# Performance work log

Measured on AMD Instinct MI355X. Metric: run time of the kernel, lower is better.

Reference implementation:

```python
import jax, jax.numpy as jnp
import numpy as np

N_FREQ = 7  # freqs = 2**linspace(0, 6, 7) == 2**arange(7)
SKIP = (4,)


def nerf_encode(p):
    # nerfstudio NeRFEncoding with include_input=True, windows_param=None
    freqs = 2.0 ** jnp.arange(N_FREQ, dtype=p.dtype)          # [7]
    scaled = (2.0 * jnp.pi) * p                               # [N,3]
    s = (scaled[..., None] * freqs).reshape(p.shape[0], -1)   # [N,21]
    enc = jnp.sin(jnp.concatenate([s, s + 0.5 * jnp.pi], axis=-1))  # [N,42] = sin | cos
    return jnp.concatenate([enc, p], axis=-1)                 # [N,45]


def _hat_pt3d(w):
    # pytorch3d hat convention (transpose of the standard skew matrix)
    x, y, z = w[:, 0], w[:, 1], w[:, 2]
    o = jnp.zeros_like(x)
    return jnp.stack([
        jnp.stack([o, z, -y], -1),
        jnp.stack([-z, o, x], -1),
        jnp.stack([y, -x, o], -1)], -2)                       # [N,3,3]


def se3_exp_map_T(screw, eps=1e-4):
    # pytorch3d.transforms.se3_exp_map(screw).permute(0, 2, 1)
    v, w = screw[:, :3], screw[:, 3:]
    ang2 = jnp.clip(jnp.sum(w * w, axis=-1), eps, None)
    ang = jnp.sqrt(ang2)
    K = _hat_pt3d(w)
    KK = jnp.matmul(K, K)
    f1 = (jnp.sin(ang) / ang)[:, None, None]
    f2 = ((1.0 - jnp.cos(ang)) / ang2)[:, None, None]
    f3 = ((ang - jnp.sin(ang)) / (ang * ang2))[:, None, None]
    I = jnp.eye(3, dtype=screw.dtype)
    R = I + f1 * K + f2 * KK       # pytorch3d (row-vector) rotation
    V = I + f2 * K + f3 * KK
    T = jnp.einsum('nij,nj->ni', V, v)
    M = jnp.zeros((screw.shape[0], 4, 4), screw.dtype)
    M = M.at[:, :3, :3].set(jnp.swapaxes(R, -1, -2))  # transpose of [[R,0],[T,1]]
    M = M.at[:, :3, 3].set(T)
    M = M.at[:, 3, 3].set(1.0)
    return M


def mlp_stem(x, Ws, bs):
    inp = x
    n = len(Ws)
    for i in range(n):
        if i in SKIP:
            x = jnp.concatenate([inp, x], axis=-1)
        x = x @ Ws[i].T + bs[i]
        x = jax.nn.relu(x)  # hidden activation; i==n-1 is out_activation (also ReLU)
    return x


def setup_inputs() -> dict:
    key = jax.random.key(0)
    ks = jax.random.split(key, 16)
    N = 524288
    d = {
        'positions': jax.random.uniform(ks[0], (N, 3), jnp.float32),
        'directions': jax.random.normal(ks[1], (N, 3), jnp.float32),
        'warp_code': jax.random.normal(ks[2], (N, 8), jnp.float32),
    }
    fan_ins = [53, 128, 128, 128, 181, 128]
    for i, fi in enumerate(fan_ins):
        d[f'W{i}'] = jax.random.normal(ks[3 + i], (128, fi), jnp.float32) / np.sqrt(fi)
        d[f'b{i}'] = jnp.zeros((128,), jnp.float32)
    d['Wr'] = jax.random.normal(ks[10], (3, 128), jnp.float32) * 1e-5
    d['br'] = jnp.zeros((3,), jnp.float32)
    d['Wv'] = jax.random.normal(ks[11], (3, 128), jnp.float32) * 1e-5
    d['bv'] = jnp.zeros((3,), jnp.float32)
    return d


def reference(positions, directions, warp_code,
              W0, b0, W1, b1, W2, b2, W3, b3, W4, b4, W5, b5,
              Wr, br, Wv, bv):
    enc = nerf_encode(positions)                                  # [N,45]
    feat = mlp_stem(jnp.concatenate([enc, warp_code], axis=-1),
                    [W0, W1, W2, W3, W4, W5], [b0, b1, b2, b3, b4, b5])  # [N,128]
    r = feat @ Wr.T + br                                          # [N,3]
    v = feat @ Wv.T + bv                                          # [N,3]
    screw = jnp.concatenate([v, r], axis=-1)                      # [N,6]
    M = se3_exp_map_T(screw)                                      # [N,4,4]
    ph = jnp.concatenate([positions, jnp.ones_like(positions[:, :1])], axis=-1)
    wp_h = jnp.einsum('nij,nj->ni', M, ph)                        # [N,4]
    wp = wp_h[:, :3] / wp_h[:, 3:]
    wp = jnp.where(jnp.isnan(wp), positions, wp)
    rots = M[:, :3, :3]
    wd = jnp.einsum('nij,nj->ni', rots, directions)
    wd = jnp.where(jnp.isnan(wd), directions, wd)
    return wp, wd
```

## Files before the change

kernel.cpp:

```cpp
#include <hip/hip_runtime.h>
#include <hip/hip_bf16.h>
#include <math.h>


typedef __bf16 bf16x8 __attribute__((ext_vector_type(8)));
typedef float  f32x4  __attribute__((ext_vector_type(4)));

#define NROWS 524288
#define BROWS 128

#define P0 0
#define P1 8192
#define P2 24576
#define P3 40960
#define P4 57344
#define P5 81920
#define PH 98304
#define PTOT 100352

#define X0_OFF   0
#define XA_OFF   16384
#define BIAS_OFF 49152
#define SC_OFF   0
#define LDS_SZ   52352

template<int KS, int FAN>
__device__ __forceinline__ float pack_val(const float* __restrict__ W, int idx)
{
    int f  = idx / (KS * 512);
    int r2 = idx % (KS * 512);
    int s  = r2 >> 9, r3 = r2 & 511, ln = r3 >> 3, j = r3 & 7;
    int col = f * 16 + (ln & 15);
    int k   = s * 32 + (ln >> 4) * 8 + j;
    if (FAN == 128) return W[col * 128 + k];
    if (FAN == 53)  return (k < 53) ? W[col * 53 + k] : 0.f;
    if (k < 53)  return W[col * 181 + k];
    if (k < 64)  return 0.f;
    return W[col * 181 + (k - 11)];
}

__global__ void pack_w(const float* __restrict__ W0, const float* __restrict__ W1,
                       const float* __restrict__ W2, const float* __restrict__ W3,
                       const float* __restrict__ W4, const float* __restrict__ W5,
                       const float* __restrict__ Wr, const float* __restrict__ Wv,
                       __bf16* __restrict__ pk)
{
    int e = blockIdx.x * 256 + threadIdx.x;
    if (e >= PTOT) return;
    float val;
    if (e >= PH) {
        int rem = e - PH;
        int s = rem >> 9, r3 = rem & 511, ln = r3 >> 3, j = r3 & 7;
        int col = ln & 15;
        int k = s * 32 + (ln >> 4) * 8 + j;
        if (col < 3)      val = Wv[col * 128 + k];
        else if (col < 6) val = Wr[(col - 3) * 128 + k];
        else              val = 0.f;
    }
    else if (e < P1) val = pack_val<2, 53 >(W0, e - P0);
    else if (e < P2) val = pack_val<4, 128>(W1, e - P1);
    else if (e < P3) val = pack_val<4, 128>(W2, e - P2);
    else if (e < P4) val = pack_val<4, 128>(W3, e - P3);
    else if (e < P5) val = pack_val<6, 181>(W4, e - P4);
    else             val = pack_val<4, 128>(W5, e - P5);
    pk[e] = (__bf16)val;
}

__device__ __forceinline__ unsigned pack_bf16_2(float a, float b) {
    union { __bf16 h; unsigned short u; } x, y;
    x.h = (__bf16)a; y.h = (__bf16)b;
    return ((unsigned)y.u << 16) | (unsigned)x.u;
}

template<int KS, int SPLIT, bool BAR1>
__device__ __forceinline__ void mlp_layer(unsigned char* smem,
    const __bf16* __restrict__ pkL, int lyr,
    int lane, int c, int g, int mfG, int nfG)
{
    f32x4 acc[2][4];
    #pragma unroll
    for (int mf = 0; mf < 2; mf++) {
        f32x4 bb = *(const f32x4*)(smem + BIAS_OFF
                                   + (lyr * 128 + mfG * 32 + mf * 16 + g * 4) * 4);
        #pragma unroll
        for (int nf = 0; nf < 4; nf++) acc[mf][nf] = bb;
    }

    const bf16x8* pW = (const bf16x8*)pkL;
    bf16x8 Wf[2][2];
    #pragma unroll
    for (int mf = 0; mf < 2; mf++)
        Wf[0][mf] = pW[((mfG * 2 + mf) * KS + 0) * 64 + lane];

    #pragma unroll
    for (int s = 0; s < KS; s++) {
        if (s + 1 < KS) {
            #pragma unroll
            for (int mf = 0; mf < 2; mf++)
                Wf[(s + 1) & 1][mf] = pW[((mfG * 2 + mf) * KS + (s + 1)) * 64 + lane];
        }
        bf16x8 Bf[4];
        {
            int base, stride, k0;
            if (s < SPLIT) { base = X0_OFF; stride = 128; k0 = s * 32; }
            else           { base = XA_OFF; stride = 256; k0 = (s - SPLIT) * 32; }
            int bc = 2 * k0 + 16 * g;
            #pragma unroll
            for (int nf = 0; nf < 4; nf++) {
                int row = nfG * 64 + nf * 16 + c;
                Bf[nf] = *(const bf16x8*)(smem + base + row * stride
                                          + (bc ^ ((row & 7) << 4)));
            }
        }
        #pragma unroll
        for (int mf = 0; mf < 2; mf++)
            #pragma unroll
            for (int nf = 0; nf < 4; nf++)
                acc[mf][nf] = __builtin_amdgcn_mfma_f32_16x16x32_bf16(
                    Wf[s & 1][mf], Bf[nf], acc[mf][nf], 0, 0, 0);
    }

    if (BAR1) __syncthreads();

    #pragma unroll
    for (int mf = 0; mf < 2; mf++)
        #pragma unroll
        for (int nf = 0; nf < 4; nf++) {
            int row = nfG * 64 + nf * 16 + c;
            int bc  = 64 * mfG + 32 * mf + 8 * g;
            f32x4 a = acc[mf][nf];
            uint2 wv;
            wv.x = pack_bf16_2(fmaxf(a[0], 0.f), fmaxf(a[1], 0.f));
            wv.y = pack_bf16_2(fmaxf(a[2], 0.f), fmaxf(a[3], 0.f));
            *(uint2*)(smem + XA_OFF + row * 256 + (bc ^ ((row & 7) << 4))) = wv;
        }
    __syncthreads();
}

__global__ __launch_bounds__(512, 6)
void se3_fused(const float* __restrict__ pos, const float* __restrict__ dir,
               const float* __restrict__ wcode,
               const float* __restrict__ b0, const float* __restrict__ b1,
               const float* __restrict__ b2, const float* __restrict__ b3,
               const float* __restrict__ b4, const float* __restrict__ b5,
               const float* __restrict__ br, const float* __restrict__ bv,
               const __bf16* __restrict__ pk,
               float* __restrict__ out)
{
    __shared__ unsigned char smem[LDS_SZ];
    const int tid  = threadIdx.x;
    const int lane = tid & 63;
    const int w    = tid >> 6;
    const int c    = lane & 15;
    const int g    = lane >> 4;
    const int mfG  = w & 3;
    const int nfG  = w >> 2;
    const int r0   = blockIdx.x * BROWS;

    if (tid < 256) {
        int row = tid >> 1, h = tid & 1;
        int gg = r0 + row;
        float p0 = pos[gg*3+0], p1 = pos[gg*3+1], p2 = pos[gg*3+2];
        float vals[32];
        if (h == 0) {
            #pragma unroll
            for (int j = 0; j < 21; j++) {
                float p = (j < 7) ? p0 : (j < 14 ? p1 : p2);
                float t = p * (float)(1 << (j % 7));
                t -= floorf(t);
                vals[j] = __sinf(6.283185307179586f * t);
            }
            #pragma unroll
            for (int j = 21; j < 32; j++) {
                int idx = j - 21;
                float p = (idx < 7) ? p0 : (idx < 14 ? p1 : p2);
                float t = p * (float)(1 << (idx % 7));
                t -= floorf(t);
                vals[j] = __cosf(6.283185307179586f * t);
            }
        } else {
            #pragma unroll
            for (int j = 0; j < 10; j++) {
                int idx = 11 + j;
                float p = (idx < 14) ? p1 : p2;
                float t = p * (float)(1 << (idx % 7));
                t -= floorf(t);
                vals[j] = __cosf(6.283185307179586f * t);
            }
            vals[10] = p0; vals[11] = p1; vals[12] = p2;
            const float4* wc4 = (const float4*)(wcode + (size_t)gg * 8);
            float4 wa = wc4[0], wb = wc4[1];
            vals[13] = wa.x; vals[14] = wa.y; vals[15] = wa.z; vals[16] = wa.w;
            vals[17] = wb.x; vals[18] = wb.y; vals[19] = wb.z; vals[20] = wb.w;
            #pragma unroll
            for (int j = 21; j < 32; j++) vals[j] = 0.f;
        }
        unsigned pkd[16];
        #pragma unroll
        for (int i = 0; i < 16; i++) pkd[i] = pack_bf16_2(vals[2*i], vals[2*i+1]);
        unsigned char* base = smem + X0_OFF + row * 128;
        int sw = (row & 7) << 4;
        #pragma unroll
        for (int cc = 0; cc < 4; cc++) {
            uint4 wv; wv.x = pkd[4*cc]; wv.y = pkd[4*cc+1];
            wv.z = pkd[4*cc+2]; wv.w = pkd[4*cc+3];
            *(uint4*)(base + ((64 * h + 16 * cc) ^ sw)) = wv;
        }
    } else {
        for (int i = tid - 256; i < 800; i += 256) {
            float v;
            if (i < 768) {
                int l = i >> 7, m = i & 127;
                const float* bp = (l == 0) ? b0 : (l == 1) ? b1 : (l == 2) ? b2
                               : (l == 3) ? b3 : (l == 4) ? b4 : b5;
                v = bp[m];
            } else {
                int m = i - 768;
                v = (m < 3) ? bv[m] : ((m < 6) ? br[m - 3] : 0.f);
            }
            *(float*)(smem + BIAS_OFF + i * 4) = v;
        }
    }
    __syncthreads();

    mlp_layer<2,2,false>(smem, pk + P0, 0, lane, c, g, mfG, nfG);
    mlp_layer<4,0,true >(smem, pk + P1, 1, lane, c, g, mfG, nfG);
    mlp_layer<4,0,true >(smem, pk + P2, 2, lane, c, g, mfG, nfG);
    mlp_layer<4,0,true >(smem, pk + P3, 3, lane, c, g, mfG, nfG);
    mlp_layer<6,2,true >(smem, pk + P4, 4, lane, c, g, mfG, nfG);
    mlp_layer<4,0,true >(smem, pk + P5, 5, lane, c, g, mfG, nfG);

    if (mfG == 0) {
        const bf16x8* pW = (const bf16x8*)(pk + PH);
        f32x4 hb = *(const f32x4*)(smem + BIAS_OFF + (768 + g * 4) * 4);
        f32x4 hacc[4];
        #pragma unroll
        for (int nf = 0; nf < 4; nf++) hacc[nf] = hb;
        #pragma unroll
        for (int s = 0; s < 4; s++) {
            bf16x8 Wh = pW[s * 64 + lane];
            int bc = 64 * s + 16 * g;
            #pragma unroll
            for (int nf = 0; nf < 4; nf++) {
                int row = nfG * 64 + nf * 16 + c;
                bf16x8 B = *(const bf16x8*)(smem + XA_OFF + row * 256
                                            + (bc ^ ((row & 7) << 4)));
                hacc[nf] = __builtin_amdgcn_mfma_f32_16x16x32_bf16(Wh, B, hacc[nf], 0, 0, 0);
            }
        }
        #pragma unroll
        for (int nf = 0; nf < 4; nf++) {
            int row = nfG * 64 + nf * 16 + c;
            if (g == 0) {
                *(f32x4*)(smem + SC_OFF + row * 32) = hacc[nf];
            } else if (g == 1) {
                float* sp = (float*)(smem + SC_OFF + row * 32);
                sp[4] = hacc[nf][0];
                sp[5] = hacc[nf][1];
            }
        }
    }
    __syncthreads();

    if (tid < BROWS) {
        int row = tid, gg = r0 + row;
        const float* sc = (const float*)(smem + SC_OFF + row * 32);
        float v0 = sc[0], v1 = sc[1], v2 = sc[2];
        float wx = sc[3], wy = sc[4], wz = sc[5];
        float ang2 = wx*wx + wy*wy + wz*wz;
        ang2 = fmaxf(ang2, 1e-4f);
        float ang = sqrtf(ang2);
        float sn = __sinf(ang), cs = __cosf(ang);
        float f1 = sn / ang;
        float f2 = (1.f - cs) / ang2;
        float f3 = (ang - sn) / (ang * ang2);
        float K[3][3] = {{0.f,  wz, -wy}, {-wz, 0.f,  wx}, { wy, -wx, 0.f}};
        float KK[3][3];
        #pragma unroll
        for (int i = 0; i < 3; i++)
            #pragma unroll
            for (int j = 0; j < 3; j++)
                KK[i][j] = K[i][0]*K[0][j] + K[i][1]*K[1][j] + K[i][2]*K[2][j];
        float R[3][3], V[3][3];
        #pragma unroll
        for (int i = 0; i < 3; i++)
            #pragma unroll
            for (int j = 0; j < 3; j++) {
                float id = (i == j) ? 1.f : 0.f;
                R[i][j] = id + f1 * K[i][j] + f2 * KK[i][j];
                V[i][j] = id + f2 * K[i][j] + f3 * KK[i][j];
            }
        float T0 = V[0][0]*v0 + V[0][1]*v1 + V[0][2]*v2;
        float T1 = V[1][0]*v0 + V[1][1]*v1 + V[1][2]*v2;
        float T2 = V[2][0]*v0 + V[2][1]*v1 + V[2][2]*v2;
        float px = pos[gg*3+0], py = pos[gg*3+1], pz = pos[gg*3+2];
        float dx = dir[gg*3+0], dy = dir[gg*3+1], dz = dir[gg*3+2];
        float wpx = R[0][0]*px + R[1][0]*py + R[2][0]*pz + T0;
        float wpy = R[0][1]*px + R[1][1]*py + R[2][1]*pz + T1;
        float wpz = R[0][2]*px + R[1][2]*py + R[2][2]*pz + T2;
        float wdx = R[0][0]*dx + R[1][0]*dy + R[2][0]*dz;
        float wdy = R[0][1]*dx + R[1][1]*dy + R[2][1]*dz;
        float wdz = R[0][2]*dx + R[1][2]*dy + R[2][2]*dz;
        wpx = (wpx != wpx) ? px : wpx;
        wpy = (wpy != wpy) ? py : wpy;
        wpz = (wpz != wpz) ? pz : wpz;
        wdx = (wdx != wdx) ? dx : wdx;
        wdy = (wdy != wdy) ? dy : wdy;
        wdz = (wdz != wdz) ? dz : wdz;
        out[gg*3+0] = wpx; out[gg*3+1] = wpy; out[gg*3+2] = wpz;
        float* o2 = out + (size_t)NROWS * 3;
        o2[gg*3+0] = wdx; o2[gg*3+1] = wdy; o2[gg*3+2] = wdz;
    }
}

extern "C" void kernel_launch(void* const* d_in, const int* in_sizes, int n_in,
                              void* d_out, int out_size, void* d_ws, size_t ws_size,
                              hipStream_t stream)
{
    const float* pos = (const float*)d_in[0];
    const float* dir = (const float*)d_in[1];
    const float* wc  = (const float*)d_in[2];
    const float* W0 = (const float*)d_in[3];  const float* b0 = (const float*)d_in[4];
    const float* W1 = (const float*)d_in[5];  const float* b1 = (const float*)d_in[6];
    const float* W2 = (const float*)d_in[7];  const float* b2 = (const float*)d_in[8];
    const float* W3 = (const float*)d_in[9];  const float* b3 = (const float*)d_in[10];
    const float* W4 = (const float*)d_in[11]; const float* b4 = (const float*)d_in[12];
    const float* W5 = (const float*)d_in[13]; const float* b5 = (const float*)d_in[14];
    const float* Wr = (const float*)d_in[15]; const float* br = (const float*)d_in[16];
    const float* Wv = (const float*)d_in[17]; const float* bv = (const float*)d_in[18];
    __bf16* pkb = (__bf16*)d_ws;
    float* out = (float*)d_out;

    pack_w<<<(PTOT + 255) / 256, 256, 0, stream>>>(W0, W1, W2, W3, W4, W5, Wr, Wv, pkb);
    se3_fused<<<NROWS / BROWS, 512, 0, stream>>>(pos, dir, wc,
                                                 b0, b1, b2, b3, b4, b5,
                                                 br, bv, pkb, out);
}
```

Measured before the change: 227.1 us.

## Switch MLP to FP8 MFMA with 256-row blocks and rescaled head weights

Moves every MLP layer and the screw head from bf16 to FP8 E4M3. Weights are packed as fp8, activations are stored to LDS as fp8, and the tiny head weights are prescaled by 4096 and unscaled afterwards. Each block now handles 256 rows, with each wave computing a 4x4 fragment tile, and the encoding uses the raw v_sin/v_cos instructions on normalized input. The goal is to halve LDS and weight bandwidth and use faster FP8 MFMA, at a large cost in precision. Outputs may drift well beyond bf16 tolerance.

```diff
diff --git a/kernel.cpp b/kernel.cpp
--- a/kernel.cpp
+++ b/kernel.cpp
@@ -1,13 +1,13 @@
 #include <hip/hip_runtime.h>
 #include <hip/hip_bf16.h>
+#include <hip/hip_fp8.h>
 #include <math.h>
 
 
-typedef __bf16 bf16x8 __attribute__((ext_vector_type(8)));
-typedef float  f32x4  __attribute__((ext_vector_type(4)));
+typedef float f32x4 __attribute__((ext_vector_type(4)));
 
 #define NROWS 524288
-#define BROWS 128
+#define BROWS 256
 
 #define P0 0
 #define P1 8192
@@ -17,6 +17,8 @@
 #define P5 81920
 #define PH 98304
 #define PTOT 100352
+
+#define QINV (1.0f / 4096.0f)
 
 #define X0_OFF   0
 #define XA_OFF   16384
@@ -43,7 +45,7 @@
                        const float* __restrict__ W2, const float* __restrict__ W3,
                        const float* __restrict__ W4, const float* __restrict__ W5,
                        const float* __restrict__ Wr, const float* __restrict__ Wv,
-                       __bf16* __restrict__ pk)
+                       unsigned char* __restrict__ pk)
 {
     int e = blockIdx.x * 256 + threadIdx.x;
     if (e >= PTOT) return;
@@ -53,8 +55,8 @@
         int s = rem >> 9, r3 = rem & 511, ln = r3 >> 3, j = r3 & 7;
         int col = ln & 15;
         int k = s * 32 + (ln >> 4) * 8 + j;
-        if (col < 3)      val = Wv[col * 128 + k];
-        else if (col < 6) val = Wr[(col - 3) * 128 + k];
+        if (col < 3)      val = Wv[col * 128 + k] * 4096.f;
+        else if (col < 6) val = Wr[(col - 3) * 128 + k] * 4096.f;
         else              val = 0.f;
     }
     else if (e < P1) val = pack_val<2, 53 >(W0, e - P0);
@@ -63,88 +65,95 @@
     else if (e < P4) val = pack_val<4, 128>(W3, e - P3);
     else if (e < P5) val = pack_val<6, 181>(W4, e - P4);
     else             val = pack_val<4, 128>(W5, e - P5);
-    pk[e] = (__bf16)val;
-}
-
-__device__ __forceinline__ unsigned pack_bf16_2(float a, float b) {
-    union { __bf16 h; unsigned short u; } x, y;
-    x.h = (__bf16)a; y.h = (__bf16)b;
-    return ((unsigned)y.u << 16) | (unsigned)x.u;
+    pk[e] = (unsigned char)__hip_cvt_float_to_fp8(val, __HIP_SATFINITE, __HIP_E4M3);
+}
+
+__device__ __forceinline__ unsigned cvt4_fp8(float a, float b, float c, float d)
+{
+#if __has_builtin(__builtin_amdgcn_cvt_pk_fp8_f32)
+    int v = __builtin_amdgcn_cvt_pk_fp8_f32(a, b, 0, false);
+    v = __builtin_amdgcn_cvt_pk_fp8_f32(c, d, v, true);
+    return (unsigned)v;
+#else
+    float2 ab; ab.x = a; ab.y = b;
+    float2 cd; cd.x = c; cd.y = d;
+    unsigned lo = (unsigned)__hip_cvt_float2_to_fp8x2(ab, __HIP_SATFINITE, __HIP_E4M3);
+    unsigned hi = (unsigned)__hip_cvt_float2_to_fp8x2(cd, __HIP_SATFINITE, __HIP_E4M3);
+    return lo | (hi << 16);
+#endif
+}
+
+__device__ __forceinline__ float fsin01(float t) {
+    float r; asm("v_sin_f32 %0, %1" : "=v"(r) : "v"(t)); return r;
+}
+__device__ __forceinline__ float fcos01(float t) {
+    float r; asm("v_cos_f32 %0, %1" : "=v"(r) : "v"(t)); return r;
 }
 
 template<int KS, int SPLIT, bool BAR1>
-__device__ __forceinline__ void mlp_layer(unsigned char* smem,
-    const __bf16* __restrict__ pkL, int lyr,
+__device__ __forceinline__ void mlp_layer(
+    unsigned char* smem, const unsigned char* __restrict__ pkL, int lyr,
+    const int* bA, const int* sB,
     int lane, int c, int g, int mfG, int nfG)
 {
-    f32x4 acc[2][4];
+    f32x4 acc[4][4];
     #pragma unroll
-    for (int mf = 0; mf < 2; mf++) {
+    for (int mf = 0; mf < 4; mf++) {
         f32x4 bb = *(const f32x4*)(smem + BIAS_OFF
-                                   + (lyr * 128 + mfG * 32 + mf * 16 + g * 4) * 4);
+                       + (lyr * 128 + mfG * 64 + mf * 16 + g * 4) * 4);
         #pragma unroll
         for (int nf = 0; nf < 4; nf++) acc[mf][nf] = bb;
     }
 
-    const bf16x8* pW = (const bf16x8*)pkL;
-    bf16x8 Wf[2][2];
-    #pragma unroll
-    for (int mf = 0; mf < 2; mf++)
-        Wf[0][mf] = pW[((mfG * 2 + mf) * KS + 0) * 64 + lane];
-
+    const unsigned long long* pA = (const unsigned long long*)pkL;
     #pragma unroll
     for (int s = 0; s < KS; s++) {
-        if (s + 1 < KS) {
-            #pragma unroll
-            for (int mf = 0; mf < 2; mf++)
-                Wf[(s + 1) & 1][mf] = pW[((mfG * 2 + mf) * KS + (s + 1)) * 64 + lane];
-        }
-        bf16x8 Bf[4];
-        {
-            int base, stride, k0;
-            if (s < SPLIT) { base = X0_OFF; stride = 128; k0 = s * 32; }
-            else           { base = XA_OFF; stride = 256; k0 = (s - SPLIT) * 32; }
-            int bc = 2 * k0 + 16 * g;
-            #pragma unroll
-            for (int nf = 0; nf < 4; nf++) {
-                int row = nfG * 64 + nf * 16 + c;
-                Bf[nf] = *(const bf16x8*)(smem + base + row * stride
-                                          + (bc ^ ((row & 7) << 4)));
-            }
-        }
-        #pragma unroll
-        for (int mf = 0; mf < 2; mf++)
+        unsigned long long Af[4];
+        #pragma unroll
+        for (int mf = 0; mf < 4; mf++)
+            Af[mf] = pA[((mfG * 4 + mf) * KS + s) * 64 + lane];
+        unsigned long long Bf[4];
+        #pragma unroll
+        for (int nf = 0; nf < 4; nf++) {
+            if (s < SPLIT) {
+                int row = 64 * nfG + 16 * nf + c;
+                Bf[nf] = *(const unsigned long long*)(smem + X0_OFF + row * 64
+                              + ((32 * s + 8 * g) ^ ((row & 7) << 3)));
+            } else {
+                Bf[nf] = *(const unsigned long long*)(smem
+                              + (bA[nf] ^ (32 * (s - SPLIT))));
+            }
+        }
+        #pragma unroll
+        for (int mf = 0; mf < 4; mf++)
             #pragma unroll
             for (int nf = 0; nf < 4; nf++)
-                acc[mf][nf] = __builtin_amdgcn_mfma_f32_16x16x32_bf16(
-                    Wf[s & 1][mf], Bf[nf], acc[mf][nf], 0, 0, 0);
+                acc[mf][nf] = __builtin_amdgcn_mfma_f32_16x16x32_fp8_fp8(
+                    (long)Af[mf], (long)Bf[nf], acc[mf][nf], 0, 0, 0);
     }
 
     if (BAR1) __syncthreads();
 
     #pragma unroll
-    for (int mf = 0; mf < 2; mf++)
+    for (int mf = 0; mf < 4; mf++)
         #pragma unroll
         for (int nf = 0; nf < 4; nf++) {
-            int row = nfG * 64 + nf * 16 + c;
-            int bc  = 64 * mfG + 32 * mf + 8 * g;
             f32x4 a = acc[mf][nf];
-            uint2 wv;
-            wv.x = pack_bf16_2(fmaxf(a[0], 0.f), fmaxf(a[1], 0.f));
-            wv.y = pack_bf16_2(fmaxf(a[2], 0.f), fmaxf(a[3], 0.f));
-            *(uint2*)(smem + XA_OFF + row * 256 + (bc ^ ((row & 7) << 4))) = wv;
+            unsigned d = cvt4_fp8(fmaxf(a[0], 0.f), fmaxf(a[1], 0.f),
+                                  fmaxf(a[2], 0.f), fmaxf(a[3], 0.f));
+            *(unsigned*)(smem + (sB[nf] ^ (16 * mf))) = d;
         }
     __syncthreads();
 }
 
-__global__ __launch_bounds__(512, 6)
+__global__ __launch_bounds__(512, 4)
 void se3_fused(const float* __restrict__ pos, const float* __restrict__ dir,
                const float* __restrict__ wcode,
                const float* __restrict__ b0, const float* __restrict__ b1,
                const float* __restrict__ b2, const float* __restrict__ b3,
                const float* __restrict__ b4, const float* __restrict__ b5,
                const float* __restrict__ br, const float* __restrict__ bv,
-               const __bf16* __restrict__ pk,
+               const unsigned char* __restrict__ pk,
                float* __restrict__ out)
 {
     __shared__ unsigned char smem[LDS_SZ];
@@ -153,11 +162,34 @@
     const int w    = tid >> 6;
     const int c    = lane & 15;
     const int g    = lane >> 4;
-    const int mfG  = w & 3;
-    const int nfG  = w >> 2;
+    const int mfG  = w & 1;
+    const int nfG  = w >> 1;
     const int r0   = blockIdx.x * BROWS;
 
-    if (tid < 256) {
+    int bA[4], sB[4];
+    #pragma unroll
+    for (int nf = 0; nf < 4; nf++) {
+        int row = 64 * nfG + 16 * nf + c;
+        int sw  = (row & 15) << 3;
+        bA[nf] = XA_OFF + row * 128 + ((8 * g) ^ (sw & 0x18)) + (sw & 0x60);
+        sB[nf] = XA_OFF + row * 128 + ((64 * mfG + 4 * g) ^ sw);
+    }
+
+    for (int i = tid; i < 800; i += 512) {
+        float v;
+        if (i < 768) {
+            int l = i >> 7, m = i & 127;
+            const float* bp = (l == 0) ? b0 : (l == 1) ? b1 : (l == 2) ? b2
+                           : (l == 3) ? b3 : (l == 4) ? b4 : b5;
+            v = bp[m];
+        } else {
+            int m = i - 768;
+            v = (m < 3) ? bv[m] : ((m < 6) ? br[m - 3] : 0.f);
+        }
+        *(float*)(smem + BIAS_OFF + i * 4) = v;
+    }
+
+    {
         int row = tid >> 1, h = tid & 1;
         int gg = r0 + row;
         float p0 = pos[gg*3+0], p1 = pos[gg*3+1], p2 = pos[gg*3+2];
@@ -168,7 +200,7 @@
                 float p = (j < 7) ? p0 : (j < 14 ? p1 : p2);
                 float t = p * (float)(1 << (j % 7));
                 t -= floorf(t);
-                vals[j] = __sinf(6.283185307179586f * t);
+                vals[j] = fsin01(t);
             }
             #pragma unroll
             for (int j = 21; j < 32; j++) {
@@ -176,7 +208,7 @@
                 float p = (idx < 7) ? p0 : (idx < 14 ? p1 : p2);
                 float t = p * (float)(1 << (idx % 7));
                 t -= floorf(t);
-                vals[j] = __cosf(6.283185307179586f * t);
+                vals[j] = fcos01(t);
             }
         } else {
             #pragma unroll
@@ -185,7 +217,7 @@
                 float p = (idx < 14) ? p1 : p2;
                 float t = p * (float)(1 << (idx % 7));
                 t -= floorf(t);
-                vals[j] = __cosf(6.283185307179586f * t);
+                vals[j] = fcos01(t);
             }
             vals[10] = p0; vals[11] = p1; vals[12] = p2;
             const float4* wc4 = (const float4*)(wcode + (size_t)gg * 8);
@@ -195,68 +227,56 @@
             #pragma unroll
             for (int j = 21; j < 32; j++) vals[j] = 0.f;
         }
-        unsigned pkd[16];
-        #pragma unroll
-        for (int i = 0; i < 16; i++) pkd[i] = pack_bf16_2(vals[2*i], vals[2*i+1]);
-        unsigned char* base = smem + X0_OFF + row * 128;
-        int sw = (row & 7) << 4;
-        #pragma unroll
-        for (int cc = 0; cc < 4; cc++) {
-            uint4 wv; wv.x = pkd[4*cc]; wv.y = pkd[4*cc+1];
-            wv.z = pkd[4*cc+2]; wv.w = pkd[4*cc+3];
-            *(uint4*)(base + ((64 * h + 16 * cc) ^ sw)) = wv;
-        }
-    } else {
-        for (int i = tid - 256; i < 800; i += 256) {
-            float v;
-            if (i < 768) {
-                int l = i >> 7, m = i & 127;
-                const float* bp = (l == 0) ? b0 : (l == 1) ? b1 : (l == 2) ? b2
-                               : (l == 3) ? b3 : (l == 4) ? b4 : b5;
-                v = bp[m];
-            } else {
-                int m = i - 768;
-                v = (m < 3) ? bv[m] : ((m < 6) ? br[m - 3] : 0.f);
-            }
-            *(float*)(smem + BIAS_OFF + i * 4) = v;
+        unsigned dw[8];
+        #pragma unroll
+        for (int q = 0; q < 8; q++)
+            dw[q] = cvt4_fp8(vals[4*q], vals[4*q+1], vals[4*q+2], vals[4*q+3]);
+        int swx = (row & 7) << 3;
+        unsigned char* base = smem + X0_OFF + row * 64;
+        #pragma unroll
+        for (int i = 0; i < 4; i++) {
+            uint2 u; u.x = dw[2*i]; u.y = dw[2*i+1];
+            *(uint2*)(base + ((32 * h + 8 * i) ^ swx)) = u;
         }
     }
     __syncthreads();
 
-    mlp_layer<2,2,false>(smem, pk + P0, 0, lane, c, g, mfG, nfG);
-    mlp_layer<4,0,true >(smem, pk + P1, 1, lane, c, g, mfG, nfG);
-    mlp_layer<4,0,true >(smem, pk + P2, 2, lane, c, g, mfG, nfG);
-    mlp_layer<4,0,true >(smem, pk + P3, 3, lane, c, g, mfG, nfG);
-    mlp_layer<6,2,true >(smem, pk + P4, 4, lane, c, g, mfG, nfG);
-    mlp_layer<4,0,true >(smem, pk + P5, 5, lane, c, g, mfG, nfG);
+    mlp_layer<2,2,false>(smem, pk + P0, 0, bA, sB, lane, c, g, mfG, nfG);
+    mlp_layer<4,0,true >(smem, pk + P1, 1, bA, sB, lane, c, g, mfG, nfG);
+    mlp_layer<4,0,true >(smem, pk + P2, 2, bA, sB, lane, c, g, mfG, nfG);
+    mlp_layer<4,0,true >(smem, pk + P3, 3, bA, sB, lane, c, g, mfG, nfG);
+    mlp_layer<6,2,true >(smem, pk + P4, 4, bA, sB, lane, c, g, mfG, nfG);
+    mlp_layer<4,0,true >(smem, pk + P5, 5, bA, sB, lane, c, g, mfG, nfG);
 
     if (mfG == 0) {
-        const bf16x8* pW = (const bf16x8*)(pk + PH);
+        const unsigned long long* pA = (const unsigned long long*)(pk + PH);
+        f32x4 ha[4];
+        #pragma unroll
+        for (int nf = 0; nf < 4; nf++) ha[nf] = f32x4{0.f, 0.f, 0.f, 0.f};
+        #pragma unroll
+        for (int s = 0; s < 4; s++) {
+            unsigned long long Ah = pA[s * 64 + lane];
+            #pragma unroll
+            for (int nf = 0; nf < 4; nf++) {
+                unsigned long long Bf = *(const unsigned long long*)(smem
+                                           + (bA[nf] ^ (32 * s)));
+                ha[nf] = __builtin_amdgcn_mfma_f32_16x16x32_fp8_fp8(
+                    (long)Ah, (long)Bf, ha[nf], 0, 0, 0);
+            }
+        }
         f32x4 hb = *(const f32x4*)(smem + BIAS_OFF + (768 + g * 4) * 4);
-        f32x4 hacc[4];
-        #pragma unroll
-        for (int nf = 0; nf < 4; nf++) hacc[nf] = hb;
-        #pragma unroll
-        for (int s = 0; s < 4; s++) {
-            bf16x8 Wh = pW[s * 64 + lane];
-            int bc = 64 * s + 16 * g;
-            #pragma unroll
-            for (int nf = 0; nf < 4; nf++) {
-                int row = nfG * 64 + nf * 16 + c;
-                bf16x8 B = *(const bf16x8*)(smem + XA_OFF + row * 256
-                                            + (bc ^ ((row & 7) << 4)));
-                hacc[nf] = __builtin_amdgcn_mfma_f32_16x16x32_bf16(Wh, B, hacc[nf], 0, 0, 0);
-            }
-        }
         #pragma unroll
         for (int nf = 0; nf < 4; nf++) {
-            int row = nfG * 64 + nf * 16 + c;
+            int row = 64 * nfG + 16 * nf + c;
             if (g == 0) {
-                *(f32x4*)(smem + SC_OFF + row * 32) = hacc[nf];
+                f32x4 sc;
+                #pragma unroll
+                for (int r = 0; r < 4; r++) sc[r] = ha[nf][r] * QINV + hb[r];
+                *(f32x4*)(smem + SC_OFF + row * 32) = sc;
             } else if (g == 1) {
                 float* sp = (float*)(smem + SC_OFF + row * 32);
-                sp[4] = hacc[nf][0];
-                sp[5] = hacc[nf][1];
+                sp[4] = ha[nf][0] * QINV + hb[0];
+                sp[5] = ha[nf][1] * QINV + hb[1];
             }
         }
     }
@@ -328,7 +348,7 @@
     const float* W5 = (const float*)d_in[13]; const float* b5 = (const float*)d_in[14];
     const float* Wr = (const float*)d_in[15]; const float* br = (const float*)d_in[16];
     const float* Wv = (const float*)d_in[17]; const float* bv = (const float*)d_in[18];
-    __bf16* pkb = (__bf16*)d_ws;
+    unsigned char* pkb = (unsigned char*)d_ws;
     float* out = (float*)d_out;
 
     pack_w<<<(PTOT + 255) / 256, 256, 0, stream>>>(W0, W1, W2, W3, W4, W5, Wr, Wv, pkb);
```

Measured after the change: 246.3 us. +8.5%, slower.
